# Performance work log

Measured on AMD Instinct MI355X. Metric: run time of the kernel, lower is better.

## Reference

```python
import jax, jax.numpy as jnp
import numpy as np

H = 512
W = 512
NSH = 4
MU_BORDER = 1.05
S_MIN = 1.0 / 30.0   # 1 / n_gaussian_max_pixels
S_MAX = 1.0 / 0.75   # 1 / n_gaussian_min_pixels
B = 8192
N = 2048


def setup_inputs() -> dict:
    key = jax.random.key(0)
    k1, k2, k3, k4, k5, k6 = jax.random.split(key, 6)
    x_bx2 = jax.random.uniform(k1, (B, 2), dtype=jnp.float32) * jnp.array([W, H], jnp.float32)
    xyz = jax.random.uniform(k2, (N, 2), dtype=jnp.float32) * 2.0 - 1.0
    features = jax.random.uniform(k3, (N, 2 * NSH + 1, 3), dtype=jnp.float32)
    opacity = 0.1 + 0.9 * jax.random.uniform(k4, (N,), dtype=jnp.float32)
    scaling = jax.random.uniform(k5, (N, 2), dtype=jnp.float32)
    rotation = jax.random.uniform(k6, (N,), dtype=jnp.float32)
    return dict(x_bx2=x_bx2, xyz=xyz, features=features, opacity=opacity,
                scaling=scaling, rotation=rotation)


def reference(x_bx2, xyz, features, opacity, scaling, rotation):
    wh = jnp.array([W, H], x_bx2.dtype)
    xnorm = x_bx2 / wh * 2.0 - 1.0                      # [b,2] in [-1,1]
    mu = jnp.clip(xyz, -1.0, 1.0) * MU_BORDER           # [n,2]
    S = jnp.clip(scaling, 0.0, 1.0) * (S_MAX - S_MIN) + S_MIN   # [n,2]
    ang = jnp.remainder(rotation, 1.0) * (2.0 * jnp.pi)  # [n]
    c = jnp.cos(ang)
    s = jnp.sin(ang)

    # pixel-space offset point - mu: [b,n,2]
    vec = (xnorm[:, None, :] - mu[None, :, :]) * 0.5 * wh
    vx = vec[..., 0]
    vy = vec[..., 1]
    # rotated: R @ v with R = [[c,-s],[s,c]]
    rx = c * vx - s * vy
    ry = s * vx + c * vy
    # scaled Mahalanobis-style squared distance
    d2 = (S[:, 0] * rx) ** 2 + (S[:, 1] * ry) ** 2       # [b,n]
    # validity test done in torch under no_grad: ||S*R*v|| < 5
    valid = jax.lax.stop_gradient(d2) < 25.0

    # unit direction point->gaussian, rotated, then angle for SH basis
    vn = jnp.sqrt(vx * vx + vy * vy)
    inv = 1.0 / (1e-10 + vn)
    nx = vx * inv
    ny = vy * inv
    rnx = c * nx - s * ny
    rny = s * nx + c * ny
    theta = jnp.arctan2(rnx, rny)                        # [b,n] (atan2(rot_x, rot_y) as in torch)

    # SH basis: [1, sin(th), cos(th), sin(2th), cos(2th), ...] -> [b,n,2*NSH+1]
    ks = jnp.arange(1, NSH + 1, dtype=theta.dtype)
    tk = theta[..., None] * ks                           # [b,n,NSH]
    sc = jnp.stack([jnp.sin(tk), jnp.cos(tk)], axis=-1).reshape(*theta.shape, 2 * NSH)
    basis = jnp.concatenate([jnp.ones_like(theta)[..., None], sc], axis=-1)

    rgb = jax.nn.sigmoid(jnp.einsum('bnm,nmc->bnc', basis, features))  # [b,n,3]
    wgt = jnp.exp(-d2) * jnp.clip(opacity, 0.0, 1.0) * valid.astype(rgb.dtype)  # [b,n]
    # accumulate_along_rays == per-ray weighted sum of rgb
    return jnp.einsum('bn,bnc->bc', wgt, rgb)            # [b,3]
```

## Files before the change

kernel.cpp:

```cpp
#include <hip/hip_runtime.h>
#include <hip/hip_fp16.h>


constexpr int   BN    = 8192;
constexpr int   NG    = 2048;
constexpr float SMIN  = 1.0f / 30.0f;
constexpr float SSPAN = (1.0f / 0.75f - 1.0f / 30.0f);
constexpr float MUSCALE = 1.05f * 256.0f;
constexpr float LOG2E = 1.44269504088896341f;
constexpr float QT    = 25.0f * 1.44269504088896341f;
constexpr float TWOPI = 6.283185307179586f;
constexpr int   BLOCK = 256;
constexpr int   RC    = 8;
constexpr int   NBLK  = BN / RC;
constexpr int   GPT   = NG / BLOCK;
constexpr int   QMAX  = 2048;

static __device__ __forceinline__ unsigned pk2h(float a, float b) {
    __half2 h = __floats2half2_rn(a, b);
    return __builtin_bit_cast(unsigned, h);
}
static __device__ __forceinline__ float2 unpk(unsigned u) {
    __half2 h = __builtin_bit_cast(__half2, u);
    return __half22float2(h);
}

__global__ __launch_bounds__(BLOCK) void splat_one(
    const float* __restrict__ xb,
    const float* __restrict__ xyz,
    const float* __restrict__ feat,
    const float* __restrict__ opac,
    const float* __restrict__ scal,
    const float* __restrict__ rot,
    float* __restrict__ out)
{
    __shared__ unsigned su0[NG], su1[NG], su2[NG];
    __shared__ float    sray[RC * 2];
    __shared__ float    sacc[RC * 3];
    __shared__ unsigned queue[QMAX];
    __shared__ int      qcnt;

    const int tid = threadIdx.x;
    const int rc  = blockIdx.x;

    if (tid == 0) qcnt = 0;
    if (tid < RC) {
        const float2 t = reinterpret_cast<const float2*>(xb)[rc * RC + tid];
        sray[2 * tid + 0] = t.x - 256.0f;
        sray[2 * tid + 1] = t.y - 256.0f;
    }
    if (tid < RC * 3) sacc[tid] = 0.0f;

    #pragma unroll
    for (int k = 0; k < GPT; ++k) {
        const int g = k * BLOCK + tid;
        const float2 xy = reinterpret_cast<const float2*>(xyz)[g];
        const float2 sc = reinterpret_cast<const float2*>(scal)[g];
        const float  rr = rot[g];
        const float mx = fminf(fmaxf(xy.x, -1.0f), 1.0f) * MUSCALE;
        const float my = fminf(fmaxf(xy.y, -1.0f), 1.0f) * MUSCALE;
        const float s0 = fminf(fmaxf(sc.x, 0.0f), 1.0f) * SSPAN + SMIN;
        const float s1 = fminf(fmaxf(sc.y, 0.0f), 1.0f) * SSPAN + SMIN;
        const float ang = (rr - floorf(rr)) * TWOPI;
        float sn, cs;
        __sincosf(ang, &sn, &cs);
        const float qsx = s0 * s0 * LOG2E;
        const float qsy = s1 * s1 * LOG2E;
        const float c2 = cs * cs, s2 = sn * sn;
        const float A  = fmaf(qsx, c2, qsy * s2);
        const float C  = fmaf(qsx, s2, qsy * c2);
        const float Bq = 2.0f * cs * sn * (qsy - qsx);
        su0[g] = pk2h(mx, my);
        su1[g] = pk2h(A, Bq);
        su2[g] = pk2h(C, 0.0f);
    }
    __syncthreads();

    float rxs[RC], rys[RC];
    #pragma unroll
    for (int i = 0; i < RC; ++i) { rxs[i] = sray[2 * i]; rys[i] = sray[2 * i + 1]; }

    #pragma unroll
    for (int k = 0; k < GPT; ++k) {
        const int g = k * BLOCK + tid;
        const float2 m  = unpk(su0[g]);
        const float2 ab = unpk(su1[g]);
        const float2 cc = unpk(su2[g]);
        #pragma unroll
        for (int i = 0; i < RC; ++i) {
            const float vx = rxs[i] - m.x;
            const float vy = rys[i] - m.y;
            const float q  = fmaf(ab.x, vx * vx,
                             fmaf(ab.y, vx * vy, cc.x * (vy * vy)));
            if (q < QT) {
                const int idx = atomicAdd(&qcnt, 1);
                if (idx < QMAX) queue[idx] = ((unsigned)g << 3) | (unsigned)i;
            }
        }
    }
    __syncthreads();

    const int n = min(qcnt, QMAX);
    for (int j = tid; j < n; j += BLOCK) {
        const unsigned e = queue[j];
        const int g = (int)(e >> 3);
        const int i = (int)(e & 7u);

        const float2 xy = reinterpret_cast<const float2*>(xyz)[g];
        const float2 sc = reinterpret_cast<const float2*>(scal)[g];
        const float  rr = rot[g];
        const float  op = fminf(fmaxf(opac[g], 0.0f), 1.0f);
        const float mx = fminf(fmaxf(xy.x, -1.0f), 1.0f) * MUSCALE;
        const float my = fminf(fmaxf(xy.y, -1.0f), 1.0f) * MUSCALE;
        const float s0 = fminf(fmaxf(sc.x, 0.0f), 1.0f) * SSPAN + SMIN;
        const float s1 = fminf(fmaxf(sc.y, 0.0f), 1.0f) * SSPAN + SMIN;
        const float ang = (rr - floorf(rr)) * TWOPI;
        const float cs = cosf(ang);
        const float sn = sinf(ang);

        const float vx = sray[2 * i + 0] - mx;
        const float vy = sray[2 * i + 1] - my;
        const float rx = fmaf(cs, vx, -sn * vy);
        const float ry = fmaf(sn, vx,  cs * vy);
        const float q  = fmaf(s0 * s0 * LOG2E, rx * rx,
                              (s1 * s1 * LOG2E) * (ry * ry));
        const float w  = exp2f(log2f(fmaxf(op, 1e-30f)) - q);

        const float iv  = rsqrtf(fmaxf(vx * vx + vy * vy, 1e-24f));
        const float s1v = rx * iv;
        const float c1v = ry * iv;
        const float s2v = 2.0f * s1v * c1v;
        const float c2v = fmaf(-2.0f * s1v, s1v, 1.0f);
        const float s3v = fmaf(s1v, c2v, c1v * s2v);
        const float c3v = fmaf(c1v, c2v, -s1v * s2v);
        const float s4v = 2.0f * s2v * c2v;
        const float c4v = fmaf(-2.0f * s2v, s2v, 1.0f);

        const float* __restrict__ fg = feat + (size_t)g * 27;
        float x0 = fg[0], x1 = fg[1], x2 = fg[2];
        x0 = fmaf(s1v, fg[3],  x0); x1 = fmaf(s1v, fg[4],  x1); x2 = fmaf(s1v, fg[5],  x2);
        x0 = fmaf(c1v, fg[6],  x0); x1 = fmaf(c1v, fg[7],  x1); x2 = fmaf(c1v, fg[8],  x2);
        x0 = fmaf(s2v, fg[9],  x0); x1 = fmaf(s2v, fg[10], x1); x2 = fmaf(s2v, fg[11], x2);
        x0 = fmaf(c2v, fg[12], x0); x1 = fmaf(c2v, fg[13], x1); x2 = fmaf(c2v, fg[14], x2);
        x0 = fmaf(s3v, fg[15], x0); x1 = fmaf(s3v, fg[16], x1); x2 = fmaf(s3v, fg[17], x2);
        x0 = fmaf(c3v, fg[18], x0); x1 = fmaf(c3v, fg[19], x1); x2 = fmaf(c3v, fg[20], x2);
        x0 = fmaf(s4v, fg[21], x0); x1 = fmaf(s4v, fg[22], x1); x2 = fmaf(s4v, fg[23], x2);
        x0 = fmaf(c4v, fg[24], x0); x1 = fmaf(c4v, fg[25], x1); x2 = fmaf(c4v, fg[26], x2);

        atomicAdd(&sacc[3 * i + 0], __fdividef(w, 1.0f + exp2f(-x0 * LOG2E)));
        atomicAdd(&sacc[3 * i + 1], __fdividef(w, 1.0f + exp2f(-x1 * LOG2E)));
        atomicAdd(&sacc[3 * i + 2], __fdividef(w, 1.0f + exp2f(-x2 * LOG2E)));
    }
    __syncthreads();

    if (tid < RC * 3)
        out[rc * (RC * 3) + tid] = sacc[tid];
}

extern "C" void kernel_launch(void* const* d_in, const int* in_sizes, int n_in,
                              void* d_out, int out_size, void* d_ws, size_t ws_size,
                              hipStream_t stream) {
    const float* xb   = (const float*)d_in[0];
    const float* xyz  = (const float*)d_in[1];
    const float* feat = (const float*)d_in[2];
    const float* opac = (const float*)d_in[3];
    const float* scal = (const float*)d_in[4];
    const float* rot  = (const float*)d_in[5];
    float* out = (float*)d_out;

    splat_one<<<dim3(NBLK), dim3(BLOCK), 0, stream>>>(
        xb, xyz, feat, opac, scal, rot, out);
}
```

Before: 15.24 us.

## Split gaussians across two blocks per ray chunk with atomic output reduction

Adds a second grid dimension that splits the gaussian set in half, so each block preprocesses and culls only half the gaussians for its 8 rays, with a smaller queue and shared memory footprint. Partial per-ray sums are combined with global atomicAdd into an output that is zeroed by a memset beforehand. Launch bounds also request 8 waves per SIMD. The aim is more parallelism and occupancy from smaller blocks of work, at the cost of an extra memset launch, duplicated per-block setup, and global atomics.

```diff
diff --git a/kernel.cpp b/kernel.cpp
--- a/kernel.cpp
+++ b/kernel.cpp
@@ -4,6 +4,8 @@
 
 constexpr int   BN    = 8192;
 constexpr int   NG    = 2048;
+constexpr int   GS    = 2;
+constexpr int   NGH   = NG / GS;
 constexpr float SMIN  = 1.0f / 30.0f;
 constexpr float SSPAN = (1.0f / 0.75f - 1.0f / 30.0f);
 constexpr float MUSCALE = 1.05f * 256.0f;
@@ -12,9 +14,8 @@
 constexpr float TWOPI = 6.283185307179586f;
 constexpr int   BLOCK = 256;
 constexpr int   RC    = 8;
-constexpr int   NBLK  = BN / RC;
-constexpr int   GPT   = NG / BLOCK;
-constexpr int   QMAX  = 2048;
+constexpr int   GPT   = NGH / BLOCK;
+constexpr int   QMAX  = 1024;
 
 static __device__ __forceinline__ unsigned pk2h(float a, float b) {
     __half2 h = __floats2half2_rn(a, b);
@@ -25,7 +26,7 @@
     return __half22float2(h);
 }
 
-__global__ __launch_bounds__(BLOCK) void splat_one(
+__global__ __launch_bounds__(BLOCK, 8) void splat_one(
     const float* __restrict__ xb,
     const float* __restrict__ xyz,
     const float* __restrict__ feat,
@@ -34,7 +35,7 @@
     const float* __restrict__ rot,
     float* __restrict__ out)
 {
-    __shared__ unsigned su0[NG], su1[NG], su2[NG];
+    __shared__ unsigned su0[NGH], su1[NGH], su2[NGH];
     __shared__ float    sray[RC * 2];
     __shared__ float    sacc[RC * 3];
     __shared__ unsigned queue[QMAX];
@@ -42,6 +43,7 @@
 
     const int tid = threadIdx.x;
     const int rc  = blockIdx.x;
+    const int g0  = blockIdx.y * NGH;
 
     if (tid == 0) qcnt = 0;
     if (tid < RC) {
@@ -53,7 +55,8 @@
 
     #pragma unroll
     for (int k = 0; k < GPT; ++k) {
-        const int g = k * BLOCK + tid;
+        const int gl = k * BLOCK + tid;
+        const int g  = g0 + gl;
         const float2 xy = reinterpret_cast<const float2*>(xyz)[g];
         const float2 sc = reinterpret_cast<const float2*>(scal)[g];
         const float  rr = rot[g];
@@ -70,9 +73,9 @@
         const float A  = fmaf(qsx, c2, qsy * s2);
         const float C  = fmaf(qsx, s2, qsy * c2);
         const float Bq = 2.0f * cs * sn * (qsy - qsx);
-        su0[g] = pk2h(mx, my);
-        su1[g] = pk2h(A, Bq);
-        su2[g] = pk2h(C, 0.0f);
+        su0[gl] = pk2h(mx, my);
+        su1[gl] = pk2h(A, Bq);
+        su2[gl] = pk2h(C, 0.0f);
     }
     __syncthreads();
 
@@ -82,10 +85,10 @@
 
     #pragma unroll
     for (int k = 0; k < GPT; ++k) {
-        const int g = k * BLOCK + tid;
-        const float2 m  = unpk(su0[g]);
-        const float2 ab = unpk(su1[g]);
-        const float2 cc = unpk(su2[g]);
+        const int gl = k * BLOCK + tid;
+        const float2 m  = unpk(su0[gl]);
+        const float2 ab = unpk(su1[gl]);
+        const float2 cc = unpk(su2[gl]);
         #pragma unroll
         for (int i = 0; i < RC; ++i) {
             const float vx = rxs[i] - m.x;
@@ -94,7 +97,7 @@
                              fmaf(ab.y, vx * vy, cc.x * (vy * vy)));
             if (q < QT) {
                 const int idx = atomicAdd(&qcnt, 1);
-                if (idx < QMAX) queue[idx] = ((unsigned)g << 3) | (unsigned)i;
+                if (idx < QMAX) queue[idx] = ((unsigned)gl << 3) | (unsigned)i;
             }
         }
     }
@@ -103,7 +106,7 @@
     const int n = min(qcnt, QMAX);
     for (int j = tid; j < n; j += BLOCK) {
         const unsigned e = queue[j];
-        const int g = (int)(e >> 3);
+        const int g = g0 + (int)(e >> 3);
         const int i = (int)(e & 7u);
 
         const float2 xy = reinterpret_cast<const float2*>(xyz)[g];
@@ -154,7 +157,7 @@
     __syncthreads();
 
     if (tid < RC * 3)
-        out[rc * (RC * 3) + tid] = sacc[tid];
+        atomicAdd(&out[rc * (RC * 3) + tid], sacc[tid]);
 }
 
 extern "C" void kernel_launch(void* const* d_in, const int* in_sizes, int n_in,
@@ -168,6 +171,7 @@
     const float* rot  = (const float*)d_in[5];
     float* out = (float*)d_out;
 
-    splat_one<<<dim3(NBLK), dim3(BLOCK), 0, stream>>>(
+    hipMemsetAsync(out, 0, (size_t)out_size * sizeof(float), stream);
+    splat_one<<<dim3(BN / RC, GS), dim3(BLOCK), 0, stream>>>(
         xb, xyz, feat, opac, scal, rot, out);
 }
```

Measured after the change: 18.61 us. 1.22x slower.
